# Performance work log

Hardware: AMD Instinct MI355X
Metric: run time of the kernel (lower is better)

Reference implementation:

```python
import jax, jax.numpy as jnp
import numpy as np

LRELU_GAIN = np.sqrt(2.0).astype(np.float32)  # apply_activation gain for leaky_relu


def setup_inputs() -> dict:
    key = jax.random.key(0)
    ks = jax.random.split(key, 8)
    N, H, W, C_in = 8, 256, 256, 128
    num_ws, w_dim, fmaps, kernel = 16, 512, 128, 3
    return {
        "x": jax.random.normal(ks[0], (N, H, W, C_in), dtype=jnp.float32),
        "dlatents": jax.random.normal(ks[1], (N, num_ws, w_dim), dtype=jnp.float32),
        "noise": jax.random.normal(ks[2], (N, H, W, 1), dtype=jnp.float32),
        "affine_w": jax.random.normal(ks[3], (w_dim, C_in), dtype=jnp.float32),
        "affine_b": jnp.ones((C_in,), dtype=jnp.float32),  # bias_init=1
        "conv_w": jax.random.normal(ks[4], (kernel, kernel, C_in, fmaps), dtype=jnp.float32),
        "conv_b": jax.random.normal(ks[5], (fmaps,), dtype=jnp.float32),
        "noise_strength": jax.random.uniform(ks[6], (1,), dtype=jnp.float32),
        "layer_idx": 5,
    }


def reference(x, dlatents, noise, affine_w, affine_b, conv_w, conv_b, noise_strength, layer_idx):
    # --- affine (equalized-lr Linear, lr_multiplier=1): s = z @ (W/sqrt(fan_in)) + b ---
    w_dim = affine_w.shape[0]
    z = dlatents[:, layer_idx]                                   # [N, w_dim]
    s = z @ (affine_w * np.float32(1.0 / np.sqrt(w_dim))) + affine_b   # [N, C_in]

    # --- equalized-lr conv weight: w * 1/sqrt(k*k*C_in) ---
    k, _, cin, cout = conv_w.shape
    w = conv_w * np.float32(1.0 / np.sqrt(k * k * cin))          # [k,k,Cin,Cout]

    # --- demodulation coefficient d[n,o] = rsqrt(sum_{k,k,i} (w*s)^2 + eps) ---
    d = jax.lax.rsqrt(jnp.einsum('hwio,ni->no', jnp.square(w), jnp.square(s)) + 1e-8)  # [N, Cout]

    # --- non-fused modconv: modulate input, shared conv, demodulate output ---
    xm = x * s[:, None, None, :]                                 # [N,H,W,Cin]
    y = jax.lax.conv_general_dilated(
        xm, w, window_strides=(1, 1), padding='SAME',
        dimension_numbers=('NHWC', 'HWIO', 'NHWC'))              # [N,H,W,Cout]
    y = y * d[:, None, None, :]

    # --- noise injection, bias, activation (leaky_relu 0.2 with sqrt(2) gain) ---
    y = y + noise_strength[0] * noise
    y = y + conv_b
    return jax.nn.leaky_relu(y, negative_slope=0.2) * LRELU_GAIN
```

## Files before the change

kernel.cpp:

```cpp
#include <hip/hip_runtime.h>

typedef unsigned short u16;
typedef unsigned int   u32;
typedef __bf16 v8bf __attribute__((ext_vector_type(8)));
typedef float  v4f  __attribute__((ext_vector_type(4)));

#define INV_SQRT_W   0.044194173824159216f
#define INV_SQRT_KKC 0.029462782549439483f
#define LRELU_GAIN   1.4142135623730951f

__device__ __forceinline__ u16 f2bf(float f) {
    u32 u = __float_as_uint(f);
    u = (u + 0x7fffu + ((u >> 16) & 1u)) >> 16;
    return (u16)u;
}

__device__ __forceinline__ void glds16(const u16* g, u16* l) {
    __builtin_amdgcn_global_load_lds(
        (const __attribute__((address_space(1))) void*)g,
        (__attribute__((address_space(3))) void*)l, 16, 0, 0);
}

__global__ void k_s(const float* __restrict__ dlat,
                    const float* __restrict__ aw,
                    const float* __restrict__ ab,
                    const int*   __restrict__ lidx,
                    float* __restrict__ s_out)
{
    const int n   = blockIdx.x;
    const int tid = threadIdx.x;
    const int i   = tid & 127, kh = tid >> 7;
    const int li  = lidx[0];
    const float* z = dlat + (n * 16 + li) * 512 + kh * 256;
    const float* a = aw + kh * 256 * 128 + i;
    float a0 = 0.f, a1 = 0.f, a2 = 0.f, a3 = 0.f;
    for (int k = 0; k < 256; k += 4) {
        a0 += z[k + 0] * a[(k + 0) * 128];
        a1 += z[k + 1] * a[(k + 1) * 128];
        a2 += z[k + 2] * a[(k + 2) * 128];
        a3 += z[k + 3] * a[(k + 3) * 128];
    }
    __shared__ float part[256];
    part[tid] = a0 + a1 + a2 + a3;
    __syncthreads();
    if (tid < 128)
        s_out[n * 128 + i] = (part[i] + part[i + 128]) * INV_SQRT_W + ab[i];
}

__global__ void k_w2(const float* __restrict__ cw, float* __restrict__ W2)
{
    const int idx = blockIdx.x * 256 + threadIdx.x;
    float acc = 0.f;
    #pragma unroll
    for (int t = 0; t < 9; ++t) {
        float w = cw[t * 16384 + idx];
        acc += w * w;
    }
    W2[idx] = acc * (INV_SQRT_KKC * INV_SQRT_KKC);
}

__global__ void k_d(const float* __restrict__ W2,
                    const float* __restrict__ s_buf,
                    float* __restrict__ d_out)
{
    const int n = blockIdx.x;
    const int o = threadIdx.x;
    __shared__ float s2[128];
    float sv = s_buf[n * 128 + o];
    s2[o] = sv * sv;
    __syncthreads();
    float acc = 1e-8f;
    #pragma unroll 4
    for (int i = 0; i < 128; ++i)
        acc += W2[i * 128 + o] * s2[i];
    d_out[n * 128 + o] = 1.0f / sqrtf(acc);
}

__global__ void k_wmod(const float* __restrict__ cw,
                       const float* __restrict__ s_buf,
                       const float* __restrict__ d_buf,
                       u16* __restrict__ wmod)
{
    const int b   = blockIdx.x;
    const int n   = b / 36;
    const int s   = b - n * 36;
    const int q4  = s / 9;
    const int r   = s - q4 * 9;
    const int tw  = r / 3, th = r - tw * 3;
    const int tap = th * 3 + tw;
    const int cibase = q4 * 32;
    const int tid = threadIdx.x;
    __shared__ float ssh[32], dsh[128];
    if (tid < 32)  ssh[tid] = s_buf[n * 128 + cibase + tid] * INV_SQRT_KKC;
    if (tid < 128) dsh[tid] = d_buf[n * 128 + tid];
    __syncthreads();
    u16* wt = wmod + ((size_t)b << 12);
    #pragma unroll
    for (int rep = 0; rep < 2; ++rep) {
        int t2   = rep * 256 + tid;
        int g    = t2 >> 7;
        int cout = t2 & 127;
        float dv = dsh[cout];
        u32 pk[4];
        #pragma unroll
        for (int jj = 0; jj < 4; ++jj) {
            int cl = g * 8 + jj * 2;
            float v0 = cw[((tap * 128 + cibase + cl) << 7) + cout]     * ssh[cl]     * dv;
            float v1 = cw[((tap * 128 + cibase + cl + 1) << 7) + cout] * ssh[cl + 1] * dv;
            pk[jj] = (u32)f2bf(v0) | ((u32)f2bf(v1) << 16);
        }
        *(uint4*)&wt[(g << 10) + (cout << 3)] = *(uint4*)pk;
    }
}

template<int T>
__device__ __forceinline__ void conv_step(const u16* __restrict__ wn,
                                          u16* __restrict__ bsh,
                                          const u16* a_base,
                                          const u16* b_lane,
                                          v8bf af[6], v4f acc[4][4],
                                          int wid, int lane)
{
    constexpr int q4 = T / 9, rr = T % 9, tw = rr / 3, th = rr % 3;
    constexpr int slot = T % 3;
    if constexpr (T < 35) asm volatile("s_waitcnt vmcnt(2)" ::: "memory");
    else                  asm volatile("s_waitcnt vmcnt(0)" ::: "memory");
    __builtin_amdgcn_s_barrier();
    asm volatile("" ::: "memory");
    v8bf bf[4];
    #pragma unroll
    for (int ni = 0; ni < 4; ++ni)
        bf[ni] = *(const v8bf*)(b_lane + slot * 4096 + ni * 128);
    if constexpr (th == 0) {
        #pragma unroll
        for (int r = 0; r < 6; ++r)
            af[r] = *(const v8bf*)(a_base + q4 * 5824 + (r * 18 + tw) * 8);
    }
    if constexpr (T + 2 < 36) {
        constexpr int ns = (T + 2) % 3;
        #pragma unroll
        for (int t = 0; t < 2; ++t) {
            int chunk = wid + (t << 2);
            glds16(wn + (T + 2) * 4096 + (chunk << 9) + (lane << 3),
                   &bsh[ns * 4096 + (chunk << 9) + (lane << 3)]);
        }
    }
    #pragma unroll
    for (int mi = 0; mi < 4; ++mi)
        #pragma unroll
        for (int ni = 0; ni < 4; ++ni)
            acc[mi][ni] = __builtin_amdgcn_mfma_f32_16x16x32_bf16(
                af[mi + th], bf[ni], acc[mi][ni], 0, 0, 0);
}

__global__ __launch_bounds__(256, 2) void k_conv(
    const float* __restrict__ x,
    const float* __restrict__ noise,
    const float* __restrict__ conv_b,
    const float* __restrict__ nstr,
    const u16*   __restrict__ wmod,
    float* __restrict__ out)
{
    __shared__ __align__(16) u16 xs[23296];
    __shared__ __align__(16) u16 bsh[12288];

    const int bid0 = blockIdx.x;
    const int bid  = ((bid0 & 7) << 9) + (bid0 >> 3);
    const int n  = bid >> 9;
    const int hb = (bid >> 4) & 31;
    const int wb = bid & 15;
    const int h0 = hb << 3, w0 = wb << 4;

    const int tid  = threadIdx.x;
    const int lane = tid & 63;
    const int wid  = tid >> 6;
    const int wm   = wid >> 1;
    const int wq   = wid & 1;
    const int lr   = lane & 15;
    const int kg   = lane >> 4;

    const float* xbase = x + ((size_t)n << 16) * 128;
    const u16* wn = wmod + (size_t)n * 147456;

    for (int t = tid; t < 2880; t += 256) {
        int g = t & 15, q = t >> 4;
        int rr_ = q / 18, cc = q - rr_ * 18;
        int gh = h0 + rr_ - 1, gw = w0 + cc - 1;
        float v0=0.f,v1=0.f,v2=0.f,v3=0.f,v4=0.f,v5=0.f,v6=0.f,v7=0.f;
        if ((unsigned)gh < 256u && (unsigned)gw < 256u) {
            const float* src = xbase + (size_t)((gh << 8) + gw) * 128 + (g << 3);
            float4 fa = *(const float4*)(src);
            float4 fb = *(const float4*)(src + 4);
            v0=fa.x; v1=fa.y; v2=fa.z; v3=fa.w; v4=fb.x; v5=fb.y; v6=fb.z; v7=fb.w;
        }
        v8bf pk;
        pk[0]=(__bf16)v0; pk[1]=(__bf16)v1; pk[2]=(__bf16)v2; pk[3]=(__bf16)v3;
        pk[4]=(__bf16)v4; pk[5]=(__bf16)v5; pk[6]=(__bf16)v6; pk[7]=(__bf16)v7;
        *(v8bf*)&xs[g * 1456 + q * 8] = pk;
    }

    #pragma unroll
    for (int s0 = 0; s0 < 2; ++s0)
        #pragma unroll
        for (int t = 0; t < 2; ++t) {
            int chunk = wid + (t << 2);
            glds16(wn + s0 * 4096 + (chunk << 9) + (lane << 3),
                   &bsh[s0 * 4096 + (chunk << 9) + (lane << 3)]);
        }

    v4f acc[4][4];
    #pragma unroll
    for (int a = 0; a < 4; ++a)
        #pragma unroll
        for (int b2 = 0; b2 < 4; ++b2) {
            v4f zz = {0.f, 0.f, 0.f, 0.f};
            acc[a][b2] = zz;
        }

    const u16* const a_base = &xs[kg * 1456 + (wm * 72 + lr) * 8];
    const u16* const b_lane = &bsh[kg * 1024 + (wq * 64 + lr) * 8];

    asm volatile("s_waitcnt lgkmcnt(0)" ::: "memory");

    v8bf af[6];
    conv_step< 0>(wn, bsh, a_base, b_lane, af, acc, wid, lane);
    conv_step< 1>(wn, bsh, a_base, b_lane, af, acc, wid, lane);
    conv_step< 2>(wn, bsh, a_base, b_lane, af, acc, wid, lane);
    conv_step< 3>(wn, bsh, a_base, b_lane, af, acc, wid, lane);
    conv_step< 4>(wn, bsh, a_base, b_lane, af, acc, wid, lane);
    conv_step< 5>(wn, bsh, a_base, b_lane, af, acc, wid, lane);
    conv_step< 6>(wn, bsh, a_base, b_lane, af, acc, wid, lane);
    conv_step< 7>(wn, bsh, a_base, b_lane, af, acc, wid, lane);
    conv_step< 8>(wn, bsh, a_base, b_lane, af, acc, wid, lane);
    conv_step< 9>(wn, bsh, a_base, b_lane, af, acc, wid, lane);
    conv_step<10>(wn, bsh, a_base, b_lane, af, acc, wid, lane);
    conv_step<11>(wn, bsh, a_base, b_lane, af, acc, wid, lane);
    conv_step<12>(wn, bsh, a_base, b_lane, af, acc, wid, lane);
    conv_step<13>(wn, bsh, a_base, b_lane, af, acc, wid, lane);
    conv_step<14>(wn, bsh, a_base, b_lane, af, acc, wid, lane);
    conv_step<15>(wn, bsh, a_base, b_lane, af, acc, wid, lane);
    conv_step<16>(wn, bsh, a_base, b_lane, af, acc, wid, lane);
    conv_step<17>(wn, bsh, a_base, b_lane, af, acc, wid, lane);
    conv_step<18>(wn, bsh, a_base, b_lane, af, acc, wid, lane);
    conv_step<19>(wn, bsh, a_base, b_lane, af, acc, wid, lane);
    conv_step<20>(wn, bsh, a_base, b_lane, af, acc, wid, lane);
    conv_step<21>(wn, bsh, a_base, b_lane, af, acc, wid, lane);
    conv_step<22>(wn, bsh, a_base, b_lane, af, acc, wid, lane);
    conv_step<23>(wn, bsh, a_base, b_lane, af, acc, wid, lane);
    conv_step<24>(wn, bsh, a_base, b_lane, af, acc, wid, lane);
    conv_step<25>(wn, bsh, a_base, b_lane, af, acc, wid, lane);
    conv_step<26>(wn, bsh, a_base, b_lane, af, acc, wid, lane);
    conv_step<27>(wn, bsh, a_base, b_lane, af, acc, wid, lane);
    conv_step<28>(wn, bsh, a_base, b_lane, af, acc, wid, lane);
    conv_step<29>(wn, bsh, a_base, b_lane, af, acc, wid, lane);
    conv_step<30>(wn, bsh, a_base, b_lane, af, acc, wid, lane);
    conv_step<31>(wn, bsh, a_base, b_lane, af, acc, wid, lane);
    conv_step<32>(wn, bsh, a_base, b_lane, af, acc, wid, lane);
    conv_step<33>(wn, bsh, a_base, b_lane, af, acc, wid, lane);
    conv_step<34>(wn, bsh, a_base, b_lane, af, acc, wid, lane);
    conv_step<35>(wn, bsh, a_base, b_lane, af, acc, wid, lane);

    const float ns = nstr[0];
    float cb4[4];
    #pragma unroll
    for (int ni = 0; ni < 4; ++ni)
        cb4[ni] = conv_b[wq * 64 + ni * 16 + lr];
    #pragma unroll
    for (int mi = 0; mi < 4; ++mi) {
        const int h = h0 + wm * 4 + mi;
        #pragma unroll
        for (int j = 0; j < 4; ++j) {
            const int w  = w0 + kg * 4 + j;
            const float nz = noise[((n << 8) + h) * 256 + w] * ns;
            float* orow = out + (size_t)((((n << 8) + h) << 8) + w) * 128;
            #pragma unroll
            for (int ni = 0; ni < 4; ++ni) {
                const int cout = wq * 64 + ni * 16 + lr;
                float v = acc[mi][ni][j] + nz + cb4[ni];
                v = (v < 0.f ? 0.2f * v : v) * LRELU_GAIN;
                orow[cout] = v;
            }
        }
    }
}

extern "C" void kernel_launch(void* const* d_in, const int* in_sizes, int n_in,
                              void* d_out, int out_size, void* d_ws, size_t ws_size,
                              hipStream_t stream) {
    const float* x     = (const float*)d_in[0];
    const float* dlat  = (const float*)d_in[1];
    const float* noise = (const float*)d_in[2];
    const float* aw    = (const float*)d_in[3];
    const float* ab    = (const float*)d_in[4];
    const float* cw    = (const float*)d_in[5];
    const float* cb    = (const float*)d_in[6];
    const float* nstr  = (const float*)d_in[7];
    const int*   lidx  = (const int*)d_in[8];
    float* out = (float*)d_out;

    float* s_buf = (float*)d_ws;
    float* d_buf = (float*)((char*)d_ws + 4096);
    float* W2    = (float*)((char*)d_ws + 8192);
    u16*   wmod  = (u16*)((char*)d_ws + 8192);

    k_w2  <<<64,  256, 0, stream>>>(cw, W2);
    k_s   <<<8,   256, 0, stream>>>(dlat, aw, ab, lidx, s_buf);
    k_d   <<<8,   128, 0, stream>>>(W2, s_buf, d_buf);
    k_wmod<<<288, 256, 0, stream>>>(cw, s_buf, d_buf, wmod);
    k_conv<<<4096,256, 0, stream>>>(x, noise, cb, nstr, wmod, out);
}
```

Baseline: 241.0 us.

## Stage input tile in two channel halves to shrink LDS for higher occupancy

The input-activation LDS tile is halved by staging only 64 input channels at a time. The second half is loaded mid-loop, after the first 18 MFMA steps. Waits on the LDS counter are added at the steps that consume each freshly staged half. The launch bound is raised from 2 to 3 blocks per CU to use the freed LDS and hide latency with more resident waves. The cost is a second staging phase inside the main loop, which stalls compute while the global loads and conversions complete.

```diff
diff --git a/kernel.cpp b/kernel.cpp
--- a/kernel.cpp
+++ b/kernel.cpp
@@ -121,20 +121,26 @@
                                           v8bf af[6], v4f acc[4][4],
                                           int wid, int lane)
 {
-    constexpr int q4 = T / 9, rr = T % 9, tw = rr / 3, th = rr % 3;
+    constexpr int q4 = T / 9, r = T % 9, tw = r / 3, th = r % 3;
     constexpr int slot = T % 3;
-    if constexpr (T < 35) asm volatile("s_waitcnt vmcnt(2)" ::: "memory");
-    else                  asm volatile("s_waitcnt vmcnt(0)" ::: "memory");
+    constexpr int hq = q4 & 1;
+    if constexpr (T == 0 || T == 18)
+        asm volatile("s_waitcnt vmcnt(2) lgkmcnt(0)" ::: "memory");
+    else if constexpr (T == 35)
+        asm volatile("s_waitcnt vmcnt(0)" ::: "memory");
+    else
+        asm volatile("s_waitcnt vmcnt(2)" ::: "memory");
     __builtin_amdgcn_s_barrier();
     asm volatile("" ::: "memory");
+
     v8bf bf[4];
     #pragma unroll
     for (int ni = 0; ni < 4; ++ni)
-        bf[ni] = *(const v8bf*)(b_lane + slot * 4096 + ni * 128);
+        bf[ni] = *(const v8bf*)(b_lane + slot * 4096 + (ni << 7));
     if constexpr (th == 0) {
         #pragma unroll
-        for (int r = 0; r < 6; ++r)
-            af[r] = *(const v8bf*)(a_base + q4 * 5824 + (r * 18 + tw) * 8);
+        for (int j = 0; j < 6; ++j)
+            af[j] = *(const v8bf*)(a_base + hq * 5792 + (j * 18 + tw) * 8);
     }
     if constexpr (T + 2 < 36) {
         constexpr int ns = (T + 2) % 3;
@@ -153,7 +159,7 @@
                 af[mi + th], bf[ni], acc[mi][ni], 0, 0, 0);
 }
 
-__global__ __launch_bounds__(256, 2) void k_conv(
+__global__ __launch_bounds__(256, 3) void k_conv(
     const float* __restrict__ x,
     const float* __restrict__ noise,
     const float* __restrict__ conv_b,
@@ -161,15 +167,15 @@
     const u16*   __restrict__ wmod,
     float* __restrict__ out)
 {
-    __shared__ __align__(16) u16 xs[23296];
+    __shared__ __align__(16) u16 xs[11584];
     __shared__ __align__(16) u16 bsh[12288];
 
     const int bid0 = blockIdx.x;
     const int bid  = ((bid0 & 7) << 9) + (bid0 >> 3);
-    const int n  = bid >> 9;
-    const int hb = (bid >> 4) & 31;
-    const int wb = bid & 15;
-    const int h0 = hb << 3, w0 = wb << 4;
+    const int n   = bid >> 9;
+    const int hb  = (bid >> 4) & 31;
+    const int wb  = bid & 15;
+    const int h0  = hb << 3, w0 = wb << 4;
 
     const int tid  = threadIdx.x;
     const int lane = tid & 63;
@@ -180,25 +186,29 @@
     const int kg   = lane >> 4;
 
     const float* xbase = x + ((size_t)n << 16) * 128;
-    const u16* wn = wmod + (size_t)n * 147456;
-
-    for (int t = tid; t < 2880; t += 256) {
-        int g = t & 15, q = t >> 4;
-        int rr_ = q / 18, cc = q - rr_ * 18;
-        int gh = h0 + rr_ - 1, gw = w0 + cc - 1;
-        float v0=0.f,v1=0.f,v2=0.f,v3=0.f,v4=0.f,v5=0.f,v6=0.f,v7=0.f;
-        if ((unsigned)gh < 256u && (unsigned)gw < 256u) {
-            const float* src = xbase + (size_t)((gh << 8) + gw) * 128 + (g << 3);
-            float4 fa = *(const float4*)(src);
-            float4 fb = *(const float4*)(src + 4);
-            v0=fa.x; v1=fa.y; v2=fa.z; v3=fa.w; v4=fb.x; v5=fb.y; v6=fb.z; v7=fb.w;
-        }
-        v8bf pk;
-        pk[0]=(__bf16)v0; pk[1]=(__bf16)v1; pk[2]=(__bf16)v2; pk[3]=(__bf16)v3;
-        pk[4]=(__bf16)v4; pk[5]=(__bf16)v5; pk[6]=(__bf16)v6; pk[7]=(__bf16)v7;
-        *(v8bf*)&xs[g * 1456 + q * 8] = pk;
-    }
-
+
+    #define STAGE_X(ph)                                                              \
+    for (int t = tid; t < 1440; t += 256) {                                          \
+        int q = t >> 3, g = t & 7;                                                   \
+        int rr_ = q / 18, cc = q - rr_ * 18;                                         \
+        int gh = h0 + rr_ - 1, gw = w0 + cc - 1;                                     \
+        float v0=0.f,v1=0.f,v2=0.f,v3=0.f,v4=0.f,v5=0.f,v6=0.f,v7=0.f;               \
+        if ((unsigned)gh < 256u && (unsigned)gw < 256u) {                            \
+            const float* src = xbase + (size_t)((gh << 8) + gw) * 128                \
+                               + (ph) * 64 + (g << 3);                               \
+            float4 fa = *(const float4*)(src);                                       \
+            float4 fb = *(const float4*)(src + 4);                                   \
+            v0=fa.x; v1=fa.y; v2=fa.z; v3=fa.w; v4=fb.x; v5=fb.y; v6=fb.z; v7=fb.w;  \
+        }                                                                            \
+        v8bf pk;                                                                     \
+        pk[0]=(__bf16)v0; pk[1]=(__bf16)v1; pk[2]=(__bf16)v2; pk[3]=(__bf16)v3;      \
+        pk[4]=(__bf16)v4; pk[5]=(__bf16)v5; pk[6]=(__bf16)v6; pk[7]=(__bf16)v7;      \
+        *(v8bf*)&xs[g * 1448 + q * 8] = pk;                                          \
+    }
+
+    STAGE_X(0)
+
+    const u16* wn = wmod + ((size_t)n * 36) * 4096;
     #pragma unroll
     for (int s0 = 0; s0 < 2; ++s0)
         #pragma unroll
@@ -217,10 +227,8 @@
             acc[a][b2] = zz;
         }
 
-    const u16* const a_base = &xs[kg * 1456 + (wm * 72 + lr) * 8];
+    const u16* const a_base = &xs[kg * 1448 + (wm * 72 + lr) * 8];
     const u16* const b_lane = &bsh[kg * 1024 + (wq * 64 + lr) * 8];
-
-    asm volatile("s_waitcnt lgkmcnt(0)" ::: "memory");
 
     v8bf af[6];
     conv_step< 0>(wn, bsh, a_base, b_lane, af, acc, wid, lane);
@@ -241,6 +249,9 @@
     conv_step<15>(wn, bsh, a_base, b_lane, af, acc, wid, lane);
     conv_step<16>(wn, bsh, a_base, b_lane, af, acc, wid, lane);
     conv_step<17>(wn, bsh, a_base, b_lane, af, acc, wid, lane);
+
+    STAGE_X(1)
+
     conv_step<18>(wn, bsh, a_base, b_lane, af, acc, wid, lane);
     conv_step<19>(wn, bsh, a_base, b_lane, af, acc, wid, lane);
     conv_step<20>(wn, bsh, a_base, b_lane, af, acc, wid, lane);
```

Result: faster. 217.6 us (-9.7%).
